# Kernel optimization log

Measured on AMD Instinct MI355X. Metric: run time of the kernel, lower is better.

Reference implementation:

```python
import jax, jax.numpy as jnp
import numpy as np

FEATURE_SIZE = (64, 64)   # (H, W)
N_REGIONS = 32
POOL = (3, 3)             # (ph, pw)
IOU_THR = 0.4
B, R, C = 4, 128, 256


def setup_inputs() -> dict:
    key = jax.random.key(0)
    kf, kx, ky, kw, kh = jax.random.split(key, 5)
    H, W = FEATURE_SIZE
    features = jax.random.normal(kf, (B, H, W, C), dtype=jnp.float32)
    # realistic RPN-style proposals in feature coordinates (x, y, w, h)
    x = jax.random.uniform(kx, (B, R), minval=0.0, maxval=W - 4.0)
    y = jax.random.uniform(ky, (B, R), minval=0.0, maxval=H - 4.0)
    w = jax.random.uniform(kw, (B, R), minval=4.0, maxval=W / 2.0)
    h = jax.random.uniform(kh, (B, R), minval=4.0, maxval=H / 2.0)
    roi = jnp.stack([x, y, w, h], axis=-1).astype(jnp.float32)
    return {"features": features, "roi": roi}


def _pairwise_iou(b):
    # b: [R, 4] xywh
    x1, y1 = b[:, 0], b[:, 1]
    x2, y2 = x1 + b[:, 2], y1 + b[:, 3]
    area = b[:, 2] * b[:, 3]
    iw = jnp.maximum(jnp.minimum(x2[:, None], x2[None, :]) - jnp.maximum(x1[:, None], x1[None, :]), 0.0)
    ih = jnp.maximum(jnp.minimum(y2[:, None], y2[None, :]) - jnp.maximum(y1[:, None], y1[None, :]), 0.0)
    inter = iw * ih
    return inter / (area[:, None] + area[None, :] - inter)


def _nms_indices(iou):
    # greedy sequential suppression: a discarded box never suppresses others
    Rn = iou.shape[0]
    j = jnp.arange(Rn)

    def body(p, keep):
        sup = keep & (j > p) & (iou[p] > IOU_THR) & keep[p]
        return keep & ~sup

    keep = jax.lax.fori_loop(0, Rn - 1, body, jnp.ones((Rn,), bool))
    # kept indices in ascending (objectness) order, padded with last index
    idx = jnp.sort(jnp.where(keep, j, Rn))[:N_REGIONS]
    return jnp.minimum(idx, Rn - 1).astype(jnp.int32)


def _clip_roi(roi):
    # roi: [B, N, 4] float xywh -> int32 [B, N, 4] xywh, clipped + min-size fixed
    H, W = FEATURE_SIZE
    x_min = jnp.maximum(0.0, roi[..., 0]).astype(jnp.int32)
    y_min = jnp.maximum(0.0, roi[..., 1]).astype(jnp.int32)
    x_max = jnp.minimum(float(W), roi[..., 0] + roi[..., 2]).astype(jnp.int32)
    y_max = jnp.minimum(float(H), roi[..., 1] + roi[..., 3]).astype(jnp.int32)

    def fix_axis(mn, mx, ps, fs):
        pad = ps - (mx - mn)
        fix_min = mn < pad // 2
        fix_max = fs - mx < (1 + pad) // 2
        sym = (pad > 0) & ~(fix_min | fix_max)
        omin = jnp.where(sym, mn - pad // 2, mn)
        omax = jnp.where(sym, mx + (1 + pad) // 2, mx)
        cmn = (pad > 0) & fix_min
        cmx = (pad > 0) & fix_max
        omin = jnp.where(cmn, 0, omin)
        omax = jnp.where(cmn, ps, omax)
        omin = jnp.where(cmx, fs - ps, omin)
        omax = jnp.where(cmx, fs, omax)
        return omin, omax

    xmn, xmx = fix_axis(x_min, x_max, POOL[1], W)
    ymn, ymx = fix_axis(y_min, y_max, POOL[0], H)
    return jnp.stack([xmn, ymn, xmx - xmn, ymx - ymn], axis=-1)


def _pool_one(feat, box):
    # feat: [H, W, C]; box: int32 [4] = (x, y, w, h); adaptive max pool to POOL
    H, W = FEATURE_SIZE
    ph, pw = POOL
    x, y, w, h = box[0], box[1], box[2], box[3]
    rows = jnp.arange(H)
    cols = jnp.arange(W)
    # cell index per row/col; last cell absorbs the remainder (matches floor steps)
    rcell = jnp.clip((rows - y) // (h // ph), 0, ph - 1)
    ccell = jnp.clip((cols - x) // (w // pw), 0, pw - 1)
    rvalid = (rows >= y) & (rows < y + h)
    cvalid = (cols >= x) & (cols < x + w)
    neg = jnp.finfo(feat.dtype).min
    f = jnp.where(rvalid[:, None, None], feat, neg)           # [H, W, C]
    rmax = jax.ops.segment_max(f, rcell, num_segments=ph)     # [ph, W, C]
    rmax = jnp.where(cvalid[None, :, None], rmax, neg)
    out = jax.ops.segment_max(jnp.swapaxes(rmax, 0, 1), ccell, num_segments=pw)  # [pw, ph, C]
    return jnp.swapaxes(out, 0, 1)                            # [ph, pw, C]


def reference(features, roi):
    iou = jax.vmap(_pairwise_iou)(roi)                         # [B, R, R]
    idx = jax.vmap(_nms_indices)(iou)                          # [B, N]
    roi_sup = jnp.take_along_axis(roi, idx[:, :, None], axis=1)  # [B, N, 4]
    roi_clipped = _clip_roi(roi_sup)                           # int32 [B, N, 4]
    pool_img = jax.vmap(_pool_one, in_axes=(None, 0))          # over regions
    pooled = jax.vmap(pool_img, in_axes=(0, 0))(features, roi_clipped)  # [B, N, ph, pw, C]
    return pooled, roi_clipped
```

## Files before the change

kernel.cpp:

```cpp
#include <hip/hip_runtime.h>
#include <float.h>

#define FH 64
#define FW 64
#define FC 256
#define NB 4
#define NR 128
#define NREG 32
#define POOLH 3
#define POOLW 3
#define IOU_THR 0.4f
#define NCELL (POOLH * POOLW)
#define MAXPIX 160

#define POOLED_ELEMS (NB * NREG * NCELL * FC)

__device__ inline void fix_axis(int mn, int mx, int ps, int fs, int& omin, int& omax) {
    int pad = ps - (mx - mn);
    bool fix_min = mn < (pad >> 1);
    bool fix_max = (fs - mx) < ((1 + pad) >> 1);
    bool sym = (pad > 0) && !(fix_min || fix_max);
    omin = sym ? (mn - (pad >> 1)) : mn;
    omax = sym ? (mx + ((1 + pad) >> 1)) : mx;
    if ((pad > 0) && fix_min) { omin = 0; omax = ps; }
    if ((pad > 0) && fix_max) { omin = fs - ps; omax = fs; }
}

__device__ inline int nth_set_bit(unsigned long long m, int r) {
    for (int i = 0; i < r; ++i) m &= (m - 1);
    return __ffsll((long long)m) - 1;
}

__device__ inline float4 max4(float4 a, float4 b) {
    float4 o;
    o.x = fmaxf(a.x, b.x); o.y = fmaxf(a.y, b.y);
    o.z = fmaxf(a.z, b.z); o.w = fmaxf(a.w, b.w);
    return o;
}

__global__ __launch_bounds__(256) void fused_kernel(
    const float* __restrict__ features,
    const float* __restrict__ roi,
    float* __restrict__ out)
{
    const int blk = blockIdx.x;
    const int reg = blk / NCELL;
    const int cell = blk - reg * NCELL;
    const int ci = cell / POOLW, cj = cell - ci * POOLW;
    const int b = reg >> 5;
    const int r = reg & 31;
    const int tid = threadIdx.x;
    const int group = tid >> 6;
    const int lane = tid & 63;

    __shared__ float sx1[NR], sy1[NR], sx2[NR], sy2[NR], sarea[NR];
    __shared__ unsigned long long smask[NR][2];
    __shared__ int sbox[4];
    __shared__ int spix[MAXPIX];
    __shared__ float4 sred[4][64];

    if (tid < NR) {
        const float4 bx = *(const float4*)(roi + ((size_t)b * NR + tid) * 4);
        sx1[tid] = bx.x; sy1[tid] = bx.y;
        sx2[tid] = bx.x + bx.z; sy2[tid] = bx.y + bx.w;
        sarea[tid] = bx.z * bx.w;
    }
    __syncthreads();

    {
        const int p = tid & 127;
        const int half = tid >> 7;
        const int j0 = half << 6;
        const float px1 = sx1[p], py1 = sy1[p], px2 = sx2[p], py2 = sy2[p], pa = sarea[p];
        unsigned long long m = 0ull;
        #pragma unroll 8
        for (int t = 0; t < 64; ++t) {
            const int j = j0 + t;
            float iw = fmaxf(fminf(px2, sx2[j]) - fmaxf(px1, sx1[j]), 0.0f);
            float ih = fmaxf(fminf(py2, sy2[j]) - fmaxf(py1, sy1[j]), 0.0f);
            float inter = iw * ih;
            bool sup = (j > p) && (inter > IOU_THR * (pa + sarea[j] - inter));
            m |= ((unsigned long long)sup) << t;
        }
        smask[p][half] = m;
    }
    __syncthreads();

    if (tid == 0) {
        unsigned long long k0 = ~0ull, k1 = ~0ull;
        unsigned long long n0 = smask[0][0], n1 = smask[0][1];
        for (int p = 0; p < NR - 1; ++p) {
            unsigned long long m0 = n0, m1 = n1;
            n0 = smask[p + 1][0]; n1 = smask[p + 1][1];
            bool kept = (p < 64) ? ((k0 >> p) & 1ull) : ((k1 >> (p - 64)) & 1ull);
            if (kept) { k0 &= ~m0; k1 &= ~m1; }
        }
        int idx = NR - 1;
        int cnt0 = __popcll(k0);
        if (r < cnt0) {
            idx = nth_set_bit(k0, r);
        } else {
            int rr = r - cnt0;
            if (rr < __popcll(k1)) idx = 64 + nth_set_bit(k1, rr);
        }
        const float* rp = roi + ((size_t)b * NR + idx) * 4;
        float x = rp[0], y = rp[1], w = rp[2], h = rp[3];
        int x_min = (int)fmaxf(0.0f, x);
        int y_min = (int)fmaxf(0.0f, y);
        int x_max = (int)fminf((float)FW, x + w);
        int y_max = (int)fminf((float)FH, y + h);
        int xmn, xmx, ymn, ymx;
        fix_axis(x_min, x_max, POOLW, FW, xmn, xmx);
        fix_axis(y_min, y_max, POOLH, FH, ymn, ymx);
        sbox[0] = xmn; sbox[1] = ymn; sbox[2] = xmx - xmn; sbox[3] = ymx - ymn;
        if (cell == 0) {
            float* orc = out + POOLED_ELEMS + ((size_t)reg) * 4;
            orc[0] = (float)xmn;
            orc[1] = (float)ymn;
            orc[2] = (float)(xmx - xmn);
            orc[3] = (float)(ymx - ymn);
        }
    }
    __syncthreads();

    const int x = sbox[0], y = sbox[1], w = sbox[2], h = sbox[3];
    const int hh = h / POOLH;
    const int ww = w / POOLW;
    const int r0 = y + ci * hh;
    const int r1 = (ci < POOLH - 1) ? (y + (ci + 1) * hh) : (y + h);
    const int c0 = x + cj * ww;
    const int c1 = (cj < POOLW - 1) ? (x + (cj + 1) * ww) : (x + w);
    const int ncols = c1 - c0;
    const int n = (r1 - r0) * ncols;

    if (tid < n) {
        int q = tid / ncols;
        int cc = tid - q * ncols;
        spix[tid] = ((r0 + q) * FW + (c0 + cc)) * FC;
    }
    __syncthreads();

    const float* fbase = features + (size_t)b * FH * FW * FC;
    const float4 negv = {-FLT_MAX, -FLT_MAX, -FLT_MAX, -FLT_MAX};
    float4 m0 = negv, m1 = negv, m2 = negv, m3 = negv;
    int k = group;
    for (; k + 12 < n; k += 16) {
        int o0 = spix[k], o1 = spix[k + 4], o2 = spix[k + 8], o3 = spix[k + 12];
        float4 v0 = ((const float4*)(fbase + o0))[lane];
        float4 v1 = ((const float4*)(fbase + o1))[lane];
        float4 v2 = ((const float4*)(fbase + o2))[lane];
        float4 v3 = ((const float4*)(fbase + o3))[lane];
        m0 = max4(m0, v0); m1 = max4(m1, v1);
        m2 = max4(m2, v2); m3 = max4(m3, v3);
    }
    for (; k < n; k += 4) {
        float4 v = ((const float4*)(fbase + spix[k]))[lane];
        m0 = max4(m0, v);
    }
    sred[group][lane] = max4(max4(m0, m1), max4(m2, m3));
    __syncthreads();

    if (tid < 64) {
        float4 a = max4(max4(sred[0][tid], sred[1][tid]),
                        max4(sred[2][tid], sred[3][tid]));
        float4* ob = (float4*)(out + ((size_t)reg * NCELL + cell) * FC);
        ob[tid] = a;
    }
}

extern "C" void kernel_launch(void* const* d_in, const int* in_sizes, int n_in,
                              void* d_out, int out_size, void* d_ws, size_t ws_size,
                              hipStream_t stream) {
    const float* features = (const float*)d_in[0];
    const float* roi = (const float*)d_in[1];
    float* out = (float*)d_out;
    (void)in_sizes; (void)n_in; (void)out_size; (void)d_ws; (void)ws_size;

    fused_kernel<<<NB * NREG * NCELL, 256, 0, stream>>>(features, roi, out);
}
```

Measured before the change: 88.03 us.

## Replace serial NMS scan with wave-uniform kept-box walk and remap blocks to batches

The 127-step single-thread suppression loop is replaced by a wavefront loop that jumps only between kept boxes using ffs, broadcasting suppression masks via readlane, and stops once 32 regions are found. Box coordinates for clipping are now read from shared memory instead of global memory. Block indices are also remapped so adjacent blocks interleave batches. This targets the serial NMS latency that every one of the 1152 blocks repeats, at the cost of readlane register traffic and a more intricate control flow.

```diff
diff --git a/kernel.cpp b/kernel.cpp
--- a/kernel.cpp
+++ b/kernel.cpp
@@ -26,11 +26,6 @@
     if ((pad > 0) && fix_max) { omin = fs - ps; omax = fs; }
 }
 
-__device__ inline int nth_set_bit(unsigned long long m, int r) {
-    for (int i = 0; i < r; ++i) m &= (m - 1);
-    return __ffsll((long long)m) - 1;
-}
-
 __device__ inline float4 max4(float4 a, float4 b) {
     float4 o;
     o.x = fmaxf(a.x, b.x); o.y = fmaxf(a.y, b.y);
@@ -38,17 +33,24 @@
     return o;
 }
 
+__device__ inline unsigned long long readlane64(unsigned long long v, int lane) {
+    unsigned lo = (unsigned)__builtin_amdgcn_readlane((int)(unsigned)v, lane);
+    unsigned hi = (unsigned)__builtin_amdgcn_readlane((int)(unsigned)(v >> 32), lane);
+    return ((unsigned long long)hi << 32) | lo;
+}
+
 __global__ __launch_bounds__(256) void fused_kernel(
     const float* __restrict__ features,
     const float* __restrict__ roi,
     float* __restrict__ out)
 {
-    const int blk = blockIdx.x;
-    const int reg = blk / NCELL;
-    const int cell = blk - reg * NCELL;
+    const int hwid = blockIdx.x;
+    const int b = (hwid >> 1) & 3;
+    const int j = (hwid >> 3) * 2 + (hwid & 1);
+    const int r = j / NCELL;
+    const int cell = j - r * NCELL;
     const int ci = cell / POOLW, cj = cell - ci * POOLW;
-    const int b = reg >> 5;
-    const int r = reg & 31;
+    const int reg = b * NREG + r;
     const int tid = threadIdx.x;
     const int group = tid >> 6;
     const int lane = tid & 63;
@@ -75,50 +77,63 @@
         unsigned long long m = 0ull;
         #pragma unroll 8
         for (int t = 0; t < 64; ++t) {
-            const int j = j0 + t;
-            float iw = fmaxf(fminf(px2, sx2[j]) - fmaxf(px1, sx1[j]), 0.0f);
-            float ih = fmaxf(fminf(py2, sy2[j]) - fmaxf(py1, sy1[j]), 0.0f);
+            const int jj = j0 + t;
+            float iw = fmaxf(fminf(px2, sx2[jj]) - fmaxf(px1, sx1[jj]), 0.0f);
+            float ih = fmaxf(fminf(py2, sy2[jj]) - fmaxf(py1, sy1[jj]), 0.0f);
             float inter = iw * ih;
-            bool sup = (j > p) && (inter > IOU_THR * (pa + sarea[j] - inter));
+            bool sup = (jj > p) && (inter > IOU_THR * (pa + sarea[jj] - inter));
             m |= ((unsigned long long)sup) << t;
         }
         smask[p][half] = m;
     }
     __syncthreads();
 
-    if (tid == 0) {
-        unsigned long long k0 = ~0ull, k1 = ~0ull;
-        unsigned long long n0 = smask[0][0], n1 = smask[0][1];
-        for (int p = 0; p < NR - 1; ++p) {
-            unsigned long long m0 = n0, m1 = n1;
-            n0 = smask[p + 1][0]; n1 = smask[p + 1][1];
-            bool kept = (p < 64) ? ((k0 >> p) & 1ull) : ((k1 >> (p - 64)) & 1ull);
-            if (kept) { k0 &= ~m0; k1 &= ~m1; }
+    if (tid < 64) {
+        const unsigned long long aLo = smask[tid][0];
+        const unsigned long long aHi = smask[tid][1];
+        const unsigned long long bHi = smask[tid + 64][1];
+
+        unsigned long long k1 = ~0ull;
+        int cnt = 0, idx = NR - 1;
+
+        unsigned long long cur = ~0ull;
+        while (cur && cnt < NREG) {
+            int p = __ffsll((unsigned long long)cur) - 1;
+            if (cnt == r) idx = p;
+            ++cnt;
+            int ps = __builtin_amdgcn_readfirstlane(p);
+            unsigned long long m0 = readlane64(aLo, ps);
+            unsigned long long m1 = readlane64(aHi, ps);
+            cur = (cur & (cur - 1)) & ~m0;
+            k1 &= ~m1;
         }
-        int idx = NR - 1;
-        int cnt0 = __popcll(k0);
-        if (r < cnt0) {
-            idx = nth_set_bit(k0, r);
-        } else {
-            int rr = r - cnt0;
-            if (rr < __popcll(k1)) idx = 64 + nth_set_bit(k1, rr);
+        cur = k1;
+        while (cur && cnt < NREG) {
+            int p = __ffsll((unsigned long long)cur) - 1;
+            if (cnt == r) idx = 64 + p;
+            ++cnt;
+            int ps = __builtin_amdgcn_readfirstlane(p);
+            unsigned long long m1 = readlane64(bHi, ps);
+            cur = (cur & (cur - 1)) & ~m1;
         }
-        const float* rp = roi + ((size_t)b * NR + idx) * 4;
-        float x = rp[0], y = rp[1], w = rp[2], h = rp[3];
-        int x_min = (int)fmaxf(0.0f, x);
-        int y_min = (int)fmaxf(0.0f, y);
-        int x_max = (int)fminf((float)FW, x + w);
-        int y_max = (int)fminf((float)FH, y + h);
-        int xmn, xmx, ymn, ymx;
-        fix_axis(x_min, x_max, POOLW, FW, xmn, xmx);
-        fix_axis(y_min, y_max, POOLH, FH, ymn, ymx);
-        sbox[0] = xmn; sbox[1] = ymn; sbox[2] = xmx - xmn; sbox[3] = ymx - ymn;
-        if (cell == 0) {
-            float* orc = out + POOLED_ELEMS + ((size_t)reg) * 4;
-            orc[0] = (float)xmn;
-            orc[1] = (float)ymn;
-            orc[2] = (float)(xmx - xmn);
-            orc[3] = (float)(ymx - ymn);
+
+        if (tid == 0) {
+            float x1 = sx1[idx], y1 = sy1[idx], x2f = sx2[idx], y2f = sy2[idx];
+            int x_min = (int)fmaxf(0.0f, x1);
+            int y_min = (int)fmaxf(0.0f, y1);
+            int x_max = (int)fminf((float)FW, x2f);
+            int y_max = (int)fminf((float)FH, y2f);
+            int xmn, xmx, ymn, ymx;
+            fix_axis(x_min, x_max, POOLW, FW, xmn, xmx);
+            fix_axis(y_min, y_max, POOLH, FH, ymn, ymx);
+            sbox[0] = xmn; sbox[1] = ymn; sbox[2] = xmx - xmn; sbox[3] = ymx - ymn;
+            if (cell == 0) {
+                float* orc = out + POOLED_ELEMS + ((size_t)reg) * 4;
+                orc[0] = (float)xmn;
+                orc[1] = (float)ymn;
+                orc[2] = (float)(xmx - xmn);
+                orc[3] = (float)(ymx - ymn);
+            }
         }
     }
     __syncthreads();
```

Result: faster. 80.24 us (-8.9%).
